# Performance work log

Hardware: AMD Instinct MI355X
Metric: run time of the kernel (lower is better)

## Reference

```python
import jax, jax.numpy as jnp
import numpy as np

NEG_SLOPE = 0.01  # nn.LeakyReLU default

def _lrelu(v):
    return jnp.where(v >= 0, v, NEG_SLOPE * v)

def setup_inputs() -> dict:
    key = jax.random.key(0)
    ks = jax.random.split(key, 12)
    B, C, T = 16, 512, 128
    s = 0.02
    d = {
        'out1': jax.random.normal(ks[0], (B, C, T), jnp.float32),
        'out2': jax.random.normal(ks[1], (B, C, T), jnp.float32),
        'out3': jax.random.normal(ks[2], (B, C, T), jnp.float32),
        'theta_w': jax.random.normal(ks[3], (C, C), jnp.float32) * s,
        'phi_w':   jax.random.normal(ks[4], (C, C), jnp.float32) * s,
        'g_w':     jax.random.normal(ks[5], (C, C), jnp.float32) * s,
        'W_w':     jax.random.normal(ks[6], (C, C), jnp.float32) * s,
        'W_b':     jax.random.normal(ks[7], (C,),  jnp.float32) * s,
        'p1_w':    jax.random.normal(ks[8], (C, C), jnp.float32) * s,
        'p2_w':    jax.random.normal(ks[9], (C, C), jnp.float32) * s,
        'p3_w':    jax.random.normal(ks[10], (1, C), jnp.float32) * s,
        'p3_b':    jax.random.normal(ks[11], (1,),  jnp.float32) * s,
        'window_size': 8,
    }
    return d

def reference(out1, out2, out3, theta_w, phi_w, g_w, W_w, W_b,
              p1_w, p2_w, p3_w, p3_b, window_size):
    B, C, T = out1.shape
    w = window_size
    # stack three encoder streams: [B, C, T, 3]
    x = jnp.stack([out1, out2, out3], axis=3)
    # left-pad time axis with zeros (new_out[:, :, w-1:, :] = out)
    padded = jnp.pad(x, ((0, 0), (0, 0), (w - 1, 0), (0, 0)))
    # sliding windows over all T timesteps at once: [B, C, T, w, 3]
    idx = jnp.arange(T)[:, None] + jnp.arange(w)[None, :]
    win = padded[:, :, idx, :]
    N = w * 3  # tokens per window
    X = win.transpose(0, 2, 1, 3, 4).reshape(B, T, C, N)  # [B,T,C,N]
    # embedded-Gaussian non-local block (1x1 convs == channel matmuls)
    theta = jnp.einsum('oc,btcn->bton', theta_w, X)
    phi   = jnp.einsum('oc,btcn->bton', phi_w, X)
    g     = jnp.einsum('oc,btcn->bton', g_w, X)
    f = jnp.einsum('bton,btom->btnm', theta, phi)   # theta^T phi
    f_div = jax.nn.softmax(f, axis=-1)
    y = jnp.einsum('btnm,btom->bton', f_div, g)
    W_y = jnp.einsum('oc,btcn->bton', W_w, y) + W_b[None, None, :, None]
    z = W_y + X                                       # residual
    # AdaptiveMaxPool2d((1,1)) over the window tokens -> [B,T,C]
    pooled = jnp.max(z, axis=-1)
    h = pooled.transpose(1, 0, 2)                     # [T,B,C]
    # projector MLP (dropout = identity at inference)
    h = _lrelu(h @ p1_w.T)
    h = _lrelu(h @ p2_w.T)
    out = _lrelu(h @ p3_w.T + p3_b)                   # [T,B,1]
    return out
```

## Files before the change

### kernel.cpp

```cpp
#include <hip/hip_runtime.h>

typedef __attribute__((ext_vector_type(8))) short short8;
typedef __attribute__((ext_vector_type(4))) float float4v;
typedef __attribute__((ext_vector_type(4))) unsigned int uint4v;
typedef __attribute__((ext_vector_type(4))) unsigned short ushort4v;

__device__ __forceinline__ float lrelu(float v) { return v >= 0.f ? v : 0.01f * v; }

__device__ __forceinline__ unsigned short f2bf(float x) {
    union { float f; unsigned u; } c; c.f = x;
    unsigned r = (c.u + 0x7FFFu + ((c.u >> 16) & 1u)) >> 16;
    return (unsigned short)r;
}
__device__ __forceinline__ float bf2f(unsigned short h) {
    union { unsigned u; float f; } c; c.u = ((unsigned)h) << 16;
    return c.f;
}

__device__ __forceinline__ void gload16(const unsigned short* g, unsigned short* l) {
    __builtin_amdgcn_global_load_lds(
        (const __attribute__((address_space(1))) unsigned int*)g,
        (__attribute__((address_space(3))) unsigned int*)l, 16, 0, 0);
}

__device__ __forceinline__ void mfma_core(
    const unsigned short* __restrict__ Ah, const unsigned short* __restrict__ Al, int lda,
    const unsigned short* __restrict__ Bh, const unsigned short* __restrict__ Bl, int ldb,
    unsigned short* lds, float4v acc[4][4], int kBeg, int kEnd) {
    const int tid = threadIdx.x;
    const int lane = tid & 63, wave = tid >> 6;
    const int wm = wave >> 1, wn = wave & 1;
    const int l15 = lane & 15, lhi = lane >> 4;
    unsigned short* LAh = lds;
    unsigned short* LAl = lds + 8192;
    unsigned short* LBh = lds + 16384;
    unsigned short* LBl = lds + 24576;

    for (int k0 = kBeg; k0 < kEnd; k0 += 64) {
#pragma unroll
        for (int tile = 0; tile < 4; ++tile) {
            const unsigned short* s = (tile == 0) ? Ah : (tile == 1) ? Al : (tile == 2) ? Bh : Bl;
            int ld = (tile < 2) ? lda : ldb;
            unsigned short* dbase = lds + tile * 8192;
#pragma unroll
            for (int it = 0; it < 4; ++it) {
                int idx = it * 256 + tid;
                int row = idx >> 3, ch = idx & 7;
                gload16(&s[row * ld + k0 + ((ch ^ (row & 7)) << 3)],
                        dbase + ((it * 256 + wave * 64) << 3));
            }
        }
        __syncthreads();
#pragma unroll
        for (int ks = 0; ks < 2; ++ks) {
            short8 ah[4], al[4], bh[4], bl[4];
#pragma unroll
            for (int m = 0; m < 4; ++m) {
                int r = wm * 64 + m * 16 + l15;
                int off = r * 64 + (((ks * 4 + lhi) ^ (r & 7)) * 8);
                ah[m] = *(const short8*)&LAh[off];
                al[m] = *(const short8*)&LAl[off];
            }
#pragma unroll
            for (int n = 0; n < 4; ++n) {
                int r = wn * 64 + n * 16 + l15;
                int off = r * 64 + (((ks * 4 + lhi) ^ (r & 7)) * 8);
                bh[n] = *(const short8*)&LBh[off];
                bl[n] = *(const short8*)&LBl[off];
            }
#pragma unroll
            for (int m = 0; m < 4; ++m)
#pragma unroll
                for (int n = 0; n < 4; ++n) {
                    acc[m][n] = __builtin_amdgcn_mfma_f32_16x16x32_bf16(ah[m], bh[n], acc[m][n], 0, 0, 0);
                    acc[m][n] = __builtin_amdgcn_mfma_f32_16x16x32_bf16(ah[m], bl[n], acc[m][n], 0, 0, 0);
                    acc[m][n] = __builtin_amdgcn_mfma_f32_16x16x32_bf16(al[m], bh[n], acc[m][n], 0, 0, 0);
                }
        }
        __syncthreads();
    }
}

__global__ __launch_bounds__(256) void k_splitw6(
    const float* __restrict__ tw, const float* __restrict__ fw,
    const float* __restrict__ gw, const float* __restrict__ ww,
    const float* __restrict__ p1w, const float* __restrict__ p2w,
    unsigned short* __restrict__ TtH, unsigned short* __restrict__ TtL,
    unsigned short* __restrict__ PtH, unsigned short* __restrict__ PtL,
    unsigned short* __restrict__ GtH, unsigned short* __restrict__ GtL,
    unsigned short* __restrict__ WwH, unsigned short* __restrict__ WwL,
    unsigned short* __restrict__ p1h, unsigned short* __restrict__ p1l,
    unsigned short* __restrict__ p2h, unsigned short* __restrict__ p2l) {
    int z = blockIdx.z;
    int i0 = blockIdx.x * 32, k0 = blockIdx.y * 32;
    int tx = threadIdx.x, ty = threadIdx.y;
    __shared__ float tile[32][33];
    if (z < 3) {
        const float* src = (z == 0) ? tw : (z == 1) ? fw : gw;
        unsigned short* dh = (z == 0) ? TtH : (z == 1) ? PtH : GtH;
        unsigned short* dl = (z == 0) ? TtL : (z == 1) ? PtL : GtL;
#pragma unroll
        for (int i = 0; i < 4; ++i)
            tile[ty + i * 8][tx] = src[(k0 + ty + i * 8) * 512 + i0 + tx];
        __syncthreads();
#pragma unroll
        for (int i = 0; i < 4; ++i) {
            int row = i0 + ty + i * 8;
            float v = tile[tx][ty + i * 8];
            unsigned short h = f2bf(v), l = f2bf(v - bf2f(h));
            int idx = row * 512 + k0 + tx;
            dh[idx] = h;
            dl[idx] = l;
        }
    } else {
        const float* src = (z == 3) ? ww : (z == 4) ? p1w : p2w;
        unsigned short* dh = (z == 3) ? WwH : (z == 4) ? p1h : p2h;
        unsigned short* dl = (z == 3) ? WwL : (z == 4) ? p1l : p2l;
#pragma unroll
        for (int i = 0; i < 4; ++i) {
            int r = k0 + ty + i * 8;
            int idx = r * 512 + i0 + tx;
            float v = src[idx];
            unsigned short h = f2bf(v), l = f2bf(v - bf2f(h));
            dh[idx] = h;
            dl[idx] = l;
        }
    }
}

__global__ __launch_bounds__(256) void k_wgemm_sk(
    const unsigned short* __restrict__ WwH, const unsigned short* __restrict__ WwL,
    const unsigned short* __restrict__ GtH, const unsigned short* __restrict__ GtL,
    const unsigned short* __restrict__ TtH, const unsigned short* __restrict__ TtL,
    const unsigned short* __restrict__ PtH, const unsigned short* __restrict__ PtL,
    float* __restrict__ Pw) {
    __shared__ unsigned short lds[32768];
    int i0 = blockIdx.y * 128, j0 = blockIdx.x * 128;
    int wg = blockIdx.z >> 2, kslice = blockIdx.z & 3;
    const unsigned short* Ah = (wg == 0 ? WwH : TtH) + i0 * 512;
    const unsigned short* Al = (wg == 0 ? WwL : TtL) + i0 * 512;
    const unsigned short* Bh = (wg == 0 ? GtH : PtH) + j0 * 512;
    const unsigned short* Bl = (wg == 0 ? GtL : PtL) + j0 * 512;
    float4v acc[4][4];
#pragma unroll
    for (int m = 0; m < 4; ++m)
#pragma unroll
        for (int n = 0; n < 4; ++n) acc[m][n] = (float4v){0.f, 0.f, 0.f, 0.f};

    mfma_core(Ah, Al, 512, Bh, Bl, 512, lds, acc, kslice * 128, kslice * 128 + 128);

    int lane = threadIdx.x & 63, wave = threadIdx.x >> 6;
    int wm = wave >> 1, wn = wave & 1, l15 = lane & 15, lhi = lane >> 4;
    int rowbase = (wg == 0) ? 512 + i0 : i0;
    float* P = Pw + kslice * 524288;
#pragma unroll
    for (int m = 0; m < 4; ++m)
#pragma unroll
        for (int n = 0; n < 4; ++n) {
            int bcol = j0 + wn * 64 + n * 16 + l15;
#pragma unroll
            for (int i = 0; i < 4; ++i) {
                int r = rowbase + wm * 64 + m * 16 + lhi * 4 + i;
                P[r * 512 + bcol] = acc[m][n][i];
            }
        }
}

template <int NPART, int MODE>
__global__ __launch_bounds__(256) void k_red(
    const float* __restrict__ P, int stride,
    unsigned short* __restrict__ Ch, unsigned short* __restrict__ Cl,
    float* __restrict__ Cf) {
    int i4 = blockIdx.x * 256 + threadIdx.x;
    float4v v = ((const float4v*)P)[i4];
#pragma unroll
    for (int p = 1; p < NPART; ++p) {
        float4v u = ((const float4v*)(P + (size_t)p * stride))[i4];
#pragma unroll
        for (int j = 0; j < 4; ++j) v[j] += u[j];
    }
    if (MODE >= 1) {
#pragma unroll
        for (int j = 0; j < 4; ++j) v[j] = lrelu(v[j]);
    }
    if (MODE == 2) {
        ((float4v*)Cf)[i4] = v;
    } else {
        ushort4v h, l;
#pragma unroll
        for (int j = 0; j < 4; ++j) {
            h[j] = f2bf(v[j]);
            l[j] = f2bf(v[j] - bf2f(h[j]));
        }
        ((ushort4v*)Ch)[i4] = h;
        ((ushort4v*)Cl)[i4] = l;
    }
}

__global__ __launch_bounds__(256) void k_splitx(const float* __restrict__ o1,
                                                const float* __restrict__ o2,
                                                const float* __restrict__ o3,
                                                unsigned short* __restrict__ Xh,
                                                unsigned short* __restrict__ Xl,
                                                float* __restrict__ Xf) {
    int z = blockIdx.z;
    int b = z / 3, k = z - b * 3;
    const float* In = (k == 0) ? o1 : ((k == 1) ? o2 : o3);
    int c0 = blockIdx.x * 32, t0 = blockIdx.y * 32;
    __shared__ float tile[32][33];
    int tx = threadIdx.x, ty = threadIdx.y;
#pragma unroll
    for (int i = 0; i < 4; ++i)
        tile[ty + i * 8][tx] = In[(b * 512 + c0 + ty + i * 8) * 128 + t0 + tx];
    __syncthreads();
#pragma unroll
    for (int i = 0; i < 4; ++i) {
        int t = t0 + ty + i * 8;
        float v = tile[tx][ty + i * 8];
        unsigned short h = f2bf(v), l = f2bf(v - bf2f(h));
        int idx = ((b * 128 + t) * 3 + k) * 512 + c0 + tx;
        Xh[idx] = h;
        Xl[idx] = l;
        Xf[idx] = v;
    }
}

__global__ __launch_bounds__(256) void k_ga(
    const unsigned short* __restrict__ Whi, const unsigned short* __restrict__ Wlo,
    const unsigned short* __restrict__ Xh, const unsigned short* __restrict__ Xl,
    unsigned short* __restrict__ Yh, unsigned short* __restrict__ Yl,
    float* __restrict__ Wg) {
    __shared__ unsigned short lds[32768];
    int bk = blockIdx.x, y = blockIdx.y;
    int b = bk / 3, kin = bk - b * 3;
    int bbase = (b * 384 + kin) * 512;
    float4v acc[4][4];
#pragma unroll
    for (int m = 0; m < 4; ++m)
#pragma unroll
        for (int n = 0; n < 4; ++n) acc[m][n] = (float4v){0.f, 0.f, 0.f, 0.f};

    mfma_core(Whi + y * 128 * 512, Wlo + y * 128 * 512, 512,
              Xh + bbase, Xl + bbase, 1536, lds, acc, 0, 512);

    int lane = threadIdx.x & 63, wave = threadIdx.x >> 6;
    int wm = wave >> 1, wn = wave & 1, l15 = lane & 15, lhi = lane >> 4;
    int wsel = y >> 2, o0 = (y & 3) * 128;
#pragma unroll
    for (int m = 0; m < 4; ++m)
#pragma unroll
        for (int n = 0; n < 4; ++n) {
            int o_in = wm * 64 + m * 16 + lhi * 4;
            int t = wn * 64 + n * 16 + l15;
            int idx = bbase + t * 1536 + o0 + o_in;
            if (wsel == 1) {
                *(float4v*)&Wg[idx] = acc[m][n];
            } else {
                ushort4v h, l;
#pragma unroll
                for (int i = 0; i < 4; ++i) {
                    float v = acc[m][n][i];
                    h[i] = f2bf(v);
                    l[i] = f2bf(v - bf2f(h[i]));
                }
                *(ushort4v*)&Yh[idx] = h;
                *(ushort4v*)&Yl[idx] = l;
            }
        }
}

__global__ __launch_bounds__(64) void k_gram3(
    const unsigned short* __restrict__ Xh, const unsigned short* __restrict__ Xl,
    const unsigned short* __restrict__ Yh, const unsigned short* __restrict__ Yl,
    float* __restrict__ D) {
    __shared__ unsigned short lds[8192];
    int orig = blockIdx.x;
    int idx = (orig & 7) * 144 + (orig >> 3);
    int mat = idx >> 3, c = idx & 7;
    int b = mat / 9, r9 = mat - b * 9, k = r9 / 3, kp = r9 - k * 3;
    const unsigned short* Ahg = Xh + (b * 384 + k) * 512;
    const unsigned short* Alg = Xl + (b * 384 + k) * 512;
    const unsigned short* Bhg = Yh + (b * 384 + kp) * 512;
    const unsigned short* Blg = Yl + (b * 384 + kp) * 512;
    int t1b = c * 16, t2b0 = c * 16 - 16;
    unsigned short* LAh = lds;
    unsigned short* LAl = lds + 1024;
    unsigned short* LBh = lds + 2048;
    unsigned short* LBl = lds + 5120;
    int tid = threadIdx.x;
    int l15 = tid & 15, lhi = tid >> 4;
    float4v acc[3];
    acc[0] = (float4v){0.f, 0.f, 0.f, 0.f};
    acc[1] = (float4v){0.f, 0.f, 0.f, 0.f};
    acc[2] = (float4v){0.f, 0.f, 0.f, 0.f};

    for (int k0 = 0; k0 < 512; k0 += 64) {
#pragma unroll
        for (int it = 0; it < 2; ++it) {
            int i2 = it * 64 + tid;
            int row = i2 >> 3, ch = i2 & 7;
            int g = (t1b + row) * 1536 + k0 + ((ch ^ (row & 7)) << 3);
            gload16(&Ahg[g], LAh + ((it * 64) << 3));
            gload16(&Alg[g], LAl + ((it * 64) << 3));
        }
#pragma unroll
        for (int it = 0; it < 6; ++it) {
            int i2 = it * 64 + tid;
            int row = i2 >> 3, ch = i2 & 7;
            int t2 = t2b0 + row;
            int t2c = t2 < 0 ? 0 : (t2 > 127 ? 127 : t2);
            int g = t2c * 1536 + k0 + ((ch ^ (row & 7)) << 3);
            gload16(&Bhg[g], LBh + ((it * 64) << 3));
            gload16(&Blg[g], LBl + ((it * 64) << 3));
        }
        __syncthreads();
#pragma unroll
        for (int ks = 0; ks < 2; ++ks) {
            int offa = l15 * 64 + (((ks * 4 + lhi) ^ (l15 & 7)) * 8);
            short8 ah = *(const short8*)&LAh[offa];
            short8 al = *(const short8*)&LAl[offa];
#pragma unroll
            for (int tl = 0; tl < 3; ++tl) {
                int rb = tl * 16 + l15;
                int offb = rb * 64 + (((ks * 4 + lhi) ^ (rb & 7)) * 8);
                short8 bh = *(const short8*)&LBh[offb];
                short8 bl = *(const short8*)&LBl[offb];
                acc[tl] = __builtin_amdgcn_mfma_f32_16x16x32_bf16(ah, bh, acc[tl], 0, 0, 0);
                acc[tl] = __builtin_amdgcn_mfma_f32_16x16x32_bf16(ah, bl, acc[tl], 0, 0, 0);
                acc[tl] = __builtin_amdgcn_mfma_f32_16x16x32_bf16(al, bh, acc[tl], 0, 0, 0);
            }
        }
        __syncthreads();
    }
    float* Dm = D + mat * 16384;
#pragma unroll
    for (int tl = 0; tl < 3; ++tl) {
        int t2base = t2b0 + tl * 16;
        if (t2base < 0 || t2base > 127) continue;
        int t2 = t2base + l15;
#pragma unroll
        for (int i = 0; i < 4; ++i) {
            int t1 = t1b + lhi * 4 + i;
            Dm[t1 * 128 + t2] = acc[tl][i];
        }
    }
}

__global__ __launch_bounds__(256) void k_mlp_sk(
    const unsigned short* __restrict__ Ahi, const unsigned short* __restrict__ Alo,
    const unsigned short* __restrict__ Bhi, const unsigned short* __restrict__ Blo,
    float* __restrict__ Pp) {
    __shared__ unsigned short lds[32768];
    int r0 = blockIdx.x * 128, o0 = blockIdx.y * 128;
    int kslice = blockIdx.z;
    float4v acc[4][4];
#pragma unroll
    for (int m = 0; m < 4; ++m)
#pragma unroll
        for (int n = 0; n < 4; ++n) acc[m][n] = (float4v){0.f, 0.f, 0.f, 0.f};

    mfma_core(Ahi + r0 * 512, Alo + r0 * 512, 512, Bhi + o0 * 512, Blo + o0 * 512, 512,
              lds, acc, kslice * 256, kslice * 256 + 256);

    int lane = threadIdx.x & 63, wave = threadIdx.x >> 6;
    int wm = wave >> 1, wn = wave & 1, l15 = lane & 15, lhi = lane >> 4;
    float* P = Pp + (size_t)kslice * 1048576;
#pragma unroll
    for (int m = 0; m < 4; ++m)
#pragma unroll
        for (int n = 0; n < 4; ++n) {
            int o = o0 + wn * 64 + n * 16 + l15;
#pragma unroll
            for (int i = 0; i < 4; ++i) {
                int r = r0 + wm * 64 + m * 16 + lhi * 4 + i;
                P[r * 512 + o] = acc[m][n][i];
            }
        }
}

__global__ __launch_bounds__(512) void k_mix(
    const float* __restrict__ Xf, const float* __restrict__ Wg,
    const float* __restrict__ D, const float* __restrict__ W_b,
    unsigned short* __restrict__ Plh, unsigned short* __restrict__ Pll) {
    int orig = blockIdx.x;
    int bid = ((orig & 7) << 6) | (orig >> 3);
    int b = bid >> 5, tg = bid & 31;
    int t0 = tg * 4;
    int tid = threadIdx.x;

    __shared__ float Pm[4][24][28];

    for (int idx = tid; idx < 4 * 576; idx += 512) {
        int dt = idx / 576, r = idx - dt * 576;
        int n = r / 24, m = r - n * 24;
        int t = t0 + dt;
        int j = n / 3, k = n - j * 3;
        int jp = m / 3, kp = m - jp * 3;
        int t1 = t - 7 + j, t2 = t - 7 + jp;
        float v = 0.f;
        if (t1 >= 0 && t2 >= 0)
            v = D[((((b * 3 + k) * 3 + kp) * 128 + t1) << 7) + t2];
        Pm[dt][n][m] = v;
    }
    __syncthreads();

    if (tid < 96) {
        int dt = tid / 24, n = tid - dt * 24;
        float mx = -1e30f;
#pragma unroll
        for (int m = 0; m < 24; ++m) mx = fmaxf(mx, Pm[dt][n][m]);
        float e[24], sum = 0.f;
#pragma unroll
        for (int m = 0; m < 24; ++m) { e[m] = __expf(Pm[dt][n][m] - mx); sum += e[m]; }
        float inv = 1.0f / sum;
#pragma unroll
        for (int m = 0; m < 24; ++m) Pm[dt][n][m] = e[m] * inv;
    }
    __syncthreads();

    int o = tid;
    float wg[33], xw[33];
#pragma unroll
    for (int s = 0; s < 11; ++s) {
        int tp = t0 - 7 + s;
#pragma unroll
        for (int k = 0; k < 3; ++k) {
            int base = (((b * 128 + tp) * 3 + k) << 9) + o;
            bool ok = (tp >= 0);
            wg[s * 3 + k] = ok ? Wg[base] : 0.f;
            xw[s * 3 + k] = ok ? Xf[base] : 0.f;
        }
    }
    float wb = W_b[o];
#pragma unroll
    for (int dt = 0; dt < 4; ++dt) {
        float pooled = -1e30f;
#pragma unroll
        for (int n = 0; n < 24; ++n) {
            float s0 = 0.f, s1 = 0.f, s2 = 0.f, s3 = 0.f;
#pragma unroll
            for (int mq = 0; mq < 6; ++mq) {
                float4 p4 = *(const float4*)&Pm[dt][n][mq * 4];
                s0 += p4.x * wg[mq * 4 + 0 + dt * 3];
                s1 += p4.y * wg[mq * 4 + 1 + dt * 3];
                s2 += p4.z * wg[mq * 4 + 2 + dt * 3];
                s3 += p4.w * wg[mq * 4 + 3 + dt * 3];
            }
            float s = ((s0 + s1) + (s2 + s3)) + wb + xw[n + dt * 3];
            pooled = fmaxf(pooled, s);
        }
        int t = t0 + dt;
        int oidx = ((t * 16 + b) << 9) + o;
        unsigned short h = f2bf(pooled), l = f2bf(pooled - bf2f(h));
        Plh[oidx] = h;
        Pll[oidx] = l;
    }
}

__global__ __launch_bounds__(256) void k_final(const float* __restrict__ H,
                                               const float* __restrict__ p3w,
                                               const float* __restrict__ p3b,
                                               float* __restrict__ out) {
    int r = blockIdx.x * 4 + (threadIdx.x >> 6);
    int lane = threadIdx.x & 63;
    const float4* h4 = (const float4*)&H[r << 9];
    const float4* w4 = (const float4*)p3w;
    float4 a1 = h4[lane], a2 = h4[lane + 64];
    float4 b1 = w4[lane], b2 = w4[lane + 64];
    float s = a1.x * b1.x + a1.y * b1.y + a1.z * b1.z + a1.w * b1.w +
              a2.x * b2.x + a2.y * b2.y + a2.z * b2.z + a2.w * b2.w;
#pragma unroll
    for (int off = 32; off; off >>= 1) s += __shfl_down(s, off, 64);
    if (lane == 0) out[r] = lrelu(s + p3b[0]);
}

extern "C" void kernel_launch(void* const* d_in, const int* in_sizes, int n_in,
                              void* d_out, int out_size, void* d_ws, size_t ws_size,
                              hipStream_t stream) {
    const float* out1 = (const float*)d_in[0];
    const float* out2 = (const float*)d_in[1];
    const float* out3 = (const float*)d_in[2];
    const float* theta_w = (const float*)d_in[3];
    const float* phi_w = (const float*)d_in[4];
    const float* g_w = (const float*)d_in[5];
    const float* W_w = (const float*)d_in[6];
    const float* W_b = (const float*)d_in[7];
    const float* p1_w = (const float*)d_in[8];
    const float* p2_w = (const float*)d_in[9];
    const float* p3_w = (const float*)d_in[10];
    const float* p3_b = (const float*)d_in[11];
    float* outp = (float*)d_out;

    char* wsb = (char*)d_ws;
    unsigned short* Whi = (unsigned short*)(wsb + 0);
    unsigned short* Wlo = (unsigned short*)(wsb + 1048576);
    unsigned short* p1h = (unsigned short*)(wsb + 2097152);
    unsigned short* p1l = (unsigned short*)(wsb + 2621440);
    unsigned short* p2h = (unsigned short*)(wsb + 3145728);
    unsigned short* p2l = (unsigned short*)(wsb + 3670016);
    unsigned short* WwH = (unsigned short*)(wsb + 4194304);
    unsigned short* WwL = (unsigned short*)(wsb + 4718592);
    unsigned short* TtH = (unsigned short*)(wsb + 5242880);
    unsigned short* TtL = (unsigned short*)(wsb + 5767168);
    unsigned short* PtH = (unsigned short*)(wsb + 6291456);
    unsigned short* PtL = (unsigned short*)(wsb + 6815744);
    unsigned short* GtH = (unsigned short*)(wsb + 7340032);
    unsigned short* GtL = (unsigned short*)(wsb + 7864320);
    unsigned short* Xh  = (unsigned short*)(wsb + 8388608);
    unsigned short* Xl  = (unsigned short*)(wsb + 14680064);
    unsigned short* Yh  = (unsigned short*)(wsb + 20971520);
    unsigned short* Yl  = (unsigned short*)(wsb + 27262976);
    float* Wg = (float*)(wsb + 33554432);
    float* D  = (float*)(wsb + 46137344);
    float* Xf = (float*)(wsb + 55574528);
    float* Pw = Wg;
    float* Pp = D;
    unsigned short* Plh = (unsigned short*)(wsb + 20971520);
    unsigned short* Pll = (unsigned short*)(wsb + 23068672);
    unsigned short* h1h = (unsigned short*)(wsb + 27262976);
    unsigned short* h1l = (unsigned short*)(wsb + 29360128);
    float* h2 = (float*)(wsb + 8388608);

    k_splitw6<<<dim3(16, 16, 6), dim3(32, 8), 0, stream>>>(
        theta_w, phi_w, g_w, W_w, p1_w, p2_w,
        TtH, TtL, PtH, PtL, GtH, GtL, WwH, WwL, p1h, p1l, p2h, p2l);
    k_splitx<<<dim3(16, 4, 48), dim3(32, 8), 0, stream>>>(out1, out2, out3, Xh, Xl, Xf);
    k_wgemm_sk<<<dim3(4, 4, 8), 256, 0, stream>>>(WwH, WwL, GtH, GtL, TtH, TtL,
                                                  PtH, PtL, Pw);
    k_red<4, 0><<<dim3(512), 256, 0, stream>>>(Pw, 524288, Whi, Wlo, nullptr);
    k_ga<<<dim3(48, 8), 256, 0, stream>>>(Whi, Wlo, Xh, Xl, Yh, Yl, Wg);
    k_gram3<<<dim3(1152), 64, 0, stream>>>(Xh, Xl, Yh, Yl, D);
    k_mix<<<dim3(512), 512, 0, stream>>>(Xf, Wg, D, W_b, Plh, Pll);
    k_mlp_sk<<<dim3(16, 4, 2), 256, 0, stream>>>(Plh, Pll, p1h, p1l, Pp);
    k_red<2, 1><<<dim3(1024), 256, 0, stream>>>(Pp, 1048576, h1h, h1l, nullptr);
    k_mlp_sk<<<dim3(16, 4, 2), 256, 0, stream>>>(h1h, h1l, p2h, p2l, Pp);
    k_red<2, 2><<<dim3(1024), 256, 0, stream>>>(Pp, 1048576, nullptr, nullptr, h2);
    k_final<<<dim3(512), 256, 0, stream>>>(h2, p3_w, p3_b, outp);
}
```

Measured before the change: 122.9 us.

## Merge weight and input split kernels; process eight timesteps per mix block

Combines the weight bf16 hi/lo split and the input split/transpose into one kernel launch with a flattened grid, removing one launch and its tail. Separately, k_mix now handles 8 timesteps per block instead of 4, which halves the grid to 256 blocks and shares the sliding-window Wg/Xf register loads across more timesteps. In exchange, k_mix uses more registers (45-element arrays) and twice the shared memory, which may lower occupancy, and the smaller grid gives less parallelism.

```diff
diff --git a/kernel.cpp b/kernel.cpp
--- a/kernel.cpp
+++ b/kernel.cpp
@@ -81,49 +81,78 @@
     }
 }
 
-__global__ __launch_bounds__(256) void k_splitw6(
+__global__ __launch_bounds__(256) void k_split_all(
     const float* __restrict__ tw, const float* __restrict__ fw,
     const float* __restrict__ gw, const float* __restrict__ ww,
     const float* __restrict__ p1w, const float* __restrict__ p2w,
+    const float* __restrict__ o1, const float* __restrict__ o2,
+    const float* __restrict__ o3,
     unsigned short* __restrict__ TtH, unsigned short* __restrict__ TtL,
     unsigned short* __restrict__ PtH, unsigned short* __restrict__ PtL,
     unsigned short* __restrict__ GtH, unsigned short* __restrict__ GtL,
     unsigned short* __restrict__ WwH, unsigned short* __restrict__ WwL,
     unsigned short* __restrict__ p1h, unsigned short* __restrict__ p1l,
-    unsigned short* __restrict__ p2h, unsigned short* __restrict__ p2l) {
-    int z = blockIdx.z;
-    int i0 = blockIdx.x * 32, k0 = blockIdx.y * 32;
+    unsigned short* __restrict__ p2h, unsigned short* __restrict__ p2l,
+    unsigned short* __restrict__ Xh, unsigned short* __restrict__ Xl,
+    float* __restrict__ Xf) {
+    int bz = blockIdx.x;
     int tx = threadIdx.x, ty = threadIdx.y;
     __shared__ float tile[32][33];
-    if (z < 3) {
-        const float* src = (z == 0) ? tw : (z == 1) ? fw : gw;
-        unsigned short* dh = (z == 0) ? TtH : (z == 1) ? PtH : GtH;
-        unsigned short* dl = (z == 0) ? TtL : (z == 1) ? PtL : GtL;
+    if (bz < 1536) {
+        int z = bz >> 8, rem = bz & 255;
+        int by = rem >> 4, bx = rem & 15;
+        int i0 = bx * 32, k0 = by * 32;
+        if (z < 3) {
+            const float* src = (z == 0) ? tw : (z == 1) ? fw : gw;
+            unsigned short* dh = (z == 0) ? TtH : (z == 1) ? PtH : GtH;
+            unsigned short* dl = (z == 0) ? TtL : (z == 1) ? PtL : GtL;
+#pragma unroll
+            for (int i = 0; i < 4; ++i)
+                tile[ty + i * 8][tx] = src[(k0 + ty + i * 8) * 512 + i0 + tx];
+            __syncthreads();
+#pragma unroll
+            for (int i = 0; i < 4; ++i) {
+                int row = i0 + ty + i * 8;
+                float v = tile[tx][ty + i * 8];
+                unsigned short h = f2bf(v), l = f2bf(v - bf2f(h));
+                int idx = row * 512 + k0 + tx;
+                dh[idx] = h;
+                dl[idx] = l;
+            }
+        } else {
+            const float* src = (z == 3) ? ww : (z == 4) ? p1w : p2w;
+            unsigned short* dh = (z == 3) ? WwH : (z == 4) ? p1h : p2h;
+            unsigned short* dl = (z == 3) ? WwL : (z == 4) ? p1l : p2l;
+#pragma unroll
+            for (int i = 0; i < 4; ++i) {
+                int r = k0 + ty + i * 8;
+                int idx = r * 512 + i0 + tx;
+                float v = src[idx];
+                unsigned short h = f2bf(v), l = f2bf(v - bf2f(h));
+                dh[idx] = h;
+                dl[idx] = l;
+            }
+        }
+    } else {
+        int r = bz - 1536;
+        int z = r >> 6, rem = r & 63;
+        int by = rem >> 4, bx = rem & 15;
+        int b = z / 3, k = z - b * 3;
+        const float* In = (k == 0) ? o1 : ((k == 1) ? o2 : o3);
+        int c0 = bx * 32, t0 = by * 32;
 #pragma unroll
         for (int i = 0; i < 4; ++i)
-            tile[ty + i * 8][tx] = src[(k0 + ty + i * 8) * 512 + i0 + tx];
+            tile[ty + i * 8][tx] = In[(b * 512 + c0 + ty + i * 8) * 128 + t0 + tx];
         __syncthreads();
 #pragma unroll
         for (int i = 0; i < 4; ++i) {
-            int row = i0 + ty + i * 8;
+            int t = t0 + ty + i * 8;
             float v = tile[tx][ty + i * 8];
             unsigned short h = f2bf(v), l = f2bf(v - bf2f(h));
-            int idx = row * 512 + k0 + tx;
-            dh[idx] = h;
-            dl[idx] = l;
-        }
-    } else {
-        const float* src = (z == 3) ? ww : (z == 4) ? p1w : p2w;
-        unsigned short* dh = (z == 3) ? WwH : (z == 4) ? p1h : p2h;
-        unsigned short* dl = (z == 3) ? WwL : (z == 4) ? p1l : p2l;
-#pragma unroll
-        for (int i = 0; i < 4; ++i) {
-            int r = k0 + ty + i * 8;
-            int idx = r * 512 + i0 + tx;
-            float v = src[idx];
-            unsigned short h = f2bf(v), l = f2bf(v - bf2f(h));
-            dh[idx] = h;
-            dl[idx] = l;
+            int idx = ((b * 128 + t) * 3 + k) * 512 + c0 + tx;
+            Xh[idx] = h;
+            Xl[idx] = l;
+            Xf[idx] = v;
         }
     }
 }
@@ -194,34 +223,6 @@
         }
         ((ushort4v*)Ch)[i4] = h;
         ((ushort4v*)Cl)[i4] = l;
-    }
-}
-
-__global__ __launch_bounds__(256) void k_splitx(const float* __restrict__ o1,
-                                                const float* __restrict__ o2,
-                                                const float* __restrict__ o3,
-                                                unsigned short* __restrict__ Xh,
-                                                unsigned short* __restrict__ Xl,
-                                                float* __restrict__ Xf) {
-    int z = blockIdx.z;
-    int b = z / 3, k = z - b * 3;
-    const float* In = (k == 0) ? o1 : ((k == 1) ? o2 : o3);
-    int c0 = blockIdx.x * 32, t0 = blockIdx.y * 32;
-    __shared__ float tile[32][33];
-    int tx = threadIdx.x, ty = threadIdx.y;
-#pragma unroll
-    for (int i = 0; i < 4; ++i)
-        tile[ty + i * 8][tx] = In[(b * 512 + c0 + ty + i * 8) * 128 + t0 + tx];
-    __syncthreads();
-#pragma unroll
-    for (int i = 0; i < 4; ++i) {
-        int t = t0 + ty + i * 8;
-        float v = tile[tx][ty + i * 8];
-        unsigned short h = f2bf(v), l = f2bf(v - bf2f(h));
-        int idx = ((b * 128 + t) * 3 + k) * 512 + c0 + tx;
-        Xh[idx] = h;
-        Xl[idx] = l;
-        Xf[idx] = v;
     }
 }
 
@@ -383,14 +384,14 @@
     const float* __restrict__ D, const float* __restrict__ W_b,
     unsigned short* __restrict__ Plh, unsigned short* __restrict__ Pll) {
     int orig = blockIdx.x;
-    int bid = ((orig & 7) << 6) | (orig >> 3);
-    int b = bid >> 5, tg = bid & 31;
-    int t0 = tg * 4;
+    int bid = ((orig & 7) << 5) | (orig >> 3);
+    int b = bid >> 4, tg = bid & 15;
+    int t0 = tg * 8;
     int tid = threadIdx.x;
 
-    __shared__ float Pm[4][24][28];
-
-    for (int idx = tid; idx < 4 * 576; idx += 512) {
+    __shared__ float Pm[8][24][28];
+
+    for (int idx = tid; idx < 8 * 576; idx += 512) {
         int dt = idx / 576, r = idx - dt * 576;
         int n = r / 24, m = r - n * 24;
         int t = t0 + dt;
@@ -404,7 +405,7 @@
     }
     __syncthreads();
 
-    if (tid < 96) {
+    if (tid < 192) {
         int dt = tid / 24, n = tid - dt * 24;
         float mx = -1e30f;
 #pragma unroll
@@ -419,9 +420,9 @@
     __syncthreads();
 
     int o = tid;
-    float wg[33], xw[33];
-#pragma unroll
-    for (int s = 0; s < 11; ++s) {
+    float wg[45], xw[45];
+#pragma unroll
+    for (int s = 0; s < 15; ++s) {
         int tp = t0 - 7 + s;
 #pragma unroll
         for (int k = 0; k < 3; ++k) {
@@ -433,7 +434,7 @@
     }
     float wb = W_b[o];
 #pragma unroll
-    for (int dt = 0; dt < 4; ++dt) {
+    for (int dt = 0; dt < 8; ++dt) {
         float pooled = -1e30f;
 #pragma unroll
         for (int n = 0; n < 24; ++n) {
@@ -521,16 +522,16 @@
     unsigned short* h1l = (unsigned short*)(wsb + 29360128);
     float* h2 = (float*)(wsb + 8388608);
 
-    k_splitw6<<<dim3(16, 16, 6), dim3(32, 8), 0, stream>>>(
-        theta_w, phi_w, g_w, W_w, p1_w, p2_w,
-        TtH, TtL, PtH, PtL, GtH, GtL, WwH, WwL, p1h, p1l, p2h, p2l);
-    k_splitx<<<dim3(16, 4, 48), dim3(32, 8), 0, stream>>>(out1, out2, out3, Xh, Xl, Xf);
+    k_split_all<<<dim3(4608), dim3(32, 8), 0, stream>>>(
+        theta_w, phi_w, g_w, W_w, p1_w, p2_w, out1, out2, out3,
+        TtH, TtL, PtH, PtL, GtH, GtL, WwH, WwL, p1h, p1l, p2h, p2l,
+        Xh, Xl, Xf);
     k_wgemm_sk<<<dim3(4, 4, 8), 256, 0, stream>>>(WwH, WwL, GtH, GtL, TtH, TtL,
                                                   PtH, PtL, Pw);
     k_red<4, 0><<<dim3(512), 256, 0, stream>>>(Pw, 524288, Whi, Wlo, nullptr);
     k_ga<<<dim3(48, 8), 256, 0, stream>>>(Whi, Wlo, Xh, Xl, Yh, Yl, Wg);
     k_gram3<<<dim3(1152), 64, 0, stream>>>(Xh, Xl, Yh, Yl, D);
-    k_mix<<<dim3(512), 512, 0, stream>>>(Xf, Wg, D, W_b, Plh, Pll);
+    k_mix<<<dim3(256), 512, 0, stream>>>(Xf, Wg, D, W_b, Plh, Pll);
     k_mlp_sk<<<dim3(16, 4, 2), 256, 0, stream>>>(Plh, Pll, p1h, p1l, Pp);
     k_red<2, 1><<<dim3(1024), 256, 0, stream>>>(Pp, 1048576, h1h, h1l, nullptr);
     k_mlp_sk<<<dim3(16, 4, 2), 256, 0, stream>>>(h1h, h1l, p2h, p2l, Pp);
```

After: 127.3 us. +3.6%, slower.
